# Kernel tuning notes

Hardware: AMD Instinct MI355X
Metric: run time of the kernel (lower is better)

The kernel has to match this reference:

```python
import jax, jax.numpy as jnp
import numpy as np
from jax import lax

NUM_STATES = 1024
NUM_OBS = 512
BATCH = 64
SEQ = 128


def setup_inputs() -> dict:
    key = jax.random.key(0)
    k1, k2, k3, k4 = jax.random.split(key, 4)
    value = jax.random.randint(k1, (BATCH, SEQ), 0, NUM_OBS)  # int observation ids
    prior_logits = jax.random.normal(k2, (NUM_STATES,), dtype=jnp.float32)
    trans_logits = jax.random.normal(k3, (NUM_STATES, NUM_STATES), dtype=jnp.float32)
    emission_logits = jax.random.normal(k4, (NUM_STATES, NUM_OBS), dtype=jnp.float32)
    return {"value": value, "prior_logits": prior_logits,
            "trans_logits": trans_logits, "emission_logits": emission_logits}


def reference(value, prior_logits, trans_logits, emission_logits):
    # Categorical(...).logits in torch is log-normalized: logits - logsumexp(logits)
    prior_ln = jax.nn.log_softmax(prior_logits)                 # [S]
    trans_ln = jax.nn.log_softmax(trans_logits, axis=-1)        # [S_from, S_to], row-normalized
    emis_ln = jax.nn.log_softmax(emission_logits, axis=-1)      # [S, V]
    transT = trans_ln.T                                         # [S_to, S_from]

    # Per-timestep emission log-likelihoods: emis_ln[:, value] -> [S, B, T] -> [T, B, S]
    e = jnp.transpose(emis_ln[:, value], (2, 1, 0))

    alpha0 = e[0] + prior_ln                                    # [B, S]

    def step(alpha, e_t):
        # alpha_new[b, j] = e_t[b, j] + logsumexp_i(transT[j, i] + alpha[b, i])
        a = e_t + jax.nn.logsumexp(transT[None, :, :] + alpha[:, None, :], axis=2)
        return a, None

    alpha_final, _ = lax.scan(step, alpha0, e[1:])
    return jax.nn.logsumexp(alpha_final, axis=1)                # [B]
```

## Files before the change

### kernel.cpp

```cpp
#include <hip/hip_runtime.h>
#include <hip/hip_bf16.h>


typedef __attribute__((ext_vector_type(8))) short short8;
typedef __attribute__((ext_vector_type(4))) float f32x4;
typedef __attribute__((ext_vector_type(4))) float float4v;
typedef __attribute__((ext_vector_type(4))) unsigned int uint4v;
typedef __attribute__((ext_vector_type(2))) unsigned int uint2v;

#define ALBUF_OFF 0x330000
#define DEEP_WS_NEED (ALBUF_OFF + 128 * 131072)

__device__ __forceinline__ float bf2f(short x) {
  unsigned u = ((unsigned)(unsigned short)x) << 16;
  return __builtin_bit_cast(float, u);
}
__device__ __forceinline__ short f2bf(float f) {
  unsigned u = __builtin_bit_cast(unsigned, f);
  u += 0x7fffu + ((u >> 16) & 1u);
  return (short)(u >> 16);
}
__device__ __forceinline__ float waveReduceMax(float v) {
  #pragma unroll
  for (int d = 1; d < 64; d <<= 1) v = fmaxf(v, __shfl_xor(v, d, 64));
  return v;
}
__device__ __forceinline__ float waveReduceSum(float v) {
  #pragma unroll
  for (int d = 1; d < 64; d <<= 1) v += __shfl_xor(v, d, 64);
  return v;
}
__device__ __forceinline__ void store_u32_coh(unsigned* p, unsigned v) {
  asm volatile("global_store_dword %0, %1, off sc0 sc1" :: "v"(p), "v"(v) : "memory");
}
__device__ __forceinline__ unsigned load_u32_coh(const unsigned* p) {
  unsigned r;
  asm volatile("global_load_dword %0, %1, off sc0 sc1\n\ts_waitcnt vmcnt(0)"
               : "=v"(r) : "v"(p) : "memory");
  return r;
}


__global__ __launch_bounds__(256) void k_rowstat(const float* __restrict__ x,
                                                 float* __restrict__ rstat) {
  __shared__ float sm[8];
  const int row = blockIdx.x;
  const float* p = x + row * 1024;
  const int tid = threadIdx.x;
  float m = -1e30f;
  for (int i = tid; i < 1024; i += 256) m = fmaxf(m, p[i]);
  m = waveReduceMax(m);
  if ((tid & 63) == 0) sm[tid >> 6] = m;
  __syncthreads();
  m = fmaxf(fmaxf(sm[0], sm[1]), fmaxf(sm[2], sm[3]));
  float s = 0.f;
  for (int i = tid; i < 1024; i += 256) s += __expf(p[i] - m);
  s = waveReduceSum(s);
  if ((tid & 63) == 0) sm[4 + (tid >> 6)] = s;
  __syncthreads();
  if (tid == 0) {
    float tot = sm[4] + sm[5] + sm[6] + sm[7];
    rstat[row * 2] = m;
    rstat[row * 2 + 1] = 1.0f / tot;
  }
}

__global__ __launch_bounds__(256) void k_fillP(const float* __restrict__ trans,
                                               const float* __restrict__ rstat,
                                               short* __restrict__ P_frag) {
  __shared__ float st[512];
  const int w = blockIdx.x, tid = threadIdx.x;
  for (int kk = 0; kk < 32; ++kk) {
    for (int idx = tid; idx < 512; idx += 256) {
      int il = idx >> 4, jl = idx & 15;
      int i = kk * 32 + il, j = w * 16 + jl;
      float m = rstat[i * 2], invs = rstat[i * 2 + 1];
      st[idx] = __expf(trans[i * 1024 + j] - m) * invs;
    }
    __syncthreads();
    for (int idx = tid; idx < 512; idx += 256) {
      int lane = idx >> 3, e = idx & 7;
      int il = ((lane >> 4) & 3) * 8 + e, jl = lane & 15;
      P_frag[w * 16384 + kk * 512 + idx] = f2bf(st[il * 16 + jl]);
    }
    __syncthreads();
  }
}

__global__ __launch_bounds__(256) void k_emis(const float* __restrict__ x,
                                              short* __restrict__ o) {
  __shared__ float sm[8];
  const int row = blockIdx.x;
  const float* p = x + row * 512;
  const int tid = threadIdx.x;
  float m = -1e30f;
  for (int i = tid; i < 512; i += 256) m = fmaxf(m, p[i]);
  m = waveReduceMax(m);
  if ((tid & 63) == 0) sm[tid >> 6] = m;
  __syncthreads();
  m = fmaxf(fmaxf(sm[0], sm[1]), fmaxf(sm[2], sm[3]));
  float s = 0.f;
  for (int i = tid; i < 512; i += 256) s += __expf(p[i] - m);
  s = waveReduceSum(s);
  if ((tid & 63) == 0) sm[4 + (tid >> 6)] = s;
  __syncthreads();
  float invs = 512.0f / (sm[4] + sm[5] + sm[6] + sm[7]);
  for (int i = tid; i < 512; i += 256)
    o[i * 1024 + row] = f2bf(__expf(p[i] - m) * invs);
}

__global__ __launch_bounds__(256) void k_prior(const float* __restrict__ x,
                                               float* __restrict__ o) {
  __shared__ float sm[8];
  const int tid = threadIdx.x;
  float m = -1e30f;
  for (int i = tid; i < 1024; i += 256) m = fmaxf(m, x[i]);
  m = waveReduceMax(m);
  if ((tid & 63) == 0) sm[tid >> 6] = m;
  __syncthreads();
  m = fmaxf(fmaxf(sm[0], sm[1]), fmaxf(sm[2], sm[3]));
  float s = 0.f;
  for (int i = tid; i < 1024; i += 256) s += __expf(x[i] - m);
  s = waveReduceSum(s);
  if ((tid & 63) == 0) sm[4 + (tid >> 6)] = s;
  __syncthreads();
  float invs = 1.0f / (sm[4] + sm[5] + sm[6] + sm[7]);
  for (int i = tid; i < 1024; i += 256) o[i] = __expf(x[i] - m) * invs;
}


#define PL(KK, OFF) asm volatile("global_load_dwordx4 %0, %1, off offset:" #OFF " sc0 sc1" \
                                 : "=v"(u[KK]) : "v"(arow) : "memory")
#define PL_ALL() do { \
  PL(0,0);    PL(1,64);   PL(2,128);  PL(3,192);  PL(4,256);  PL(5,320);  PL(6,384);  PL(7,448); \
  PL(8,512);  PL(9,576);  PL(10,640); PL(11,704); PL(12,768); PL(13,832); PL(14,896); PL(15,960); \
  PL(16,1024);PL(17,1088);PL(18,1152);PL(19,1216);PL(20,1280);PL(21,1344);PL(22,1408);PL(23,1472); \
  PL(24,1536);PL(25,1600);PL(26,1664);PL(27,1728);PL(28,1792);PL(29,1856);PL(30,1920);PL(31,1984); \
  asm volatile("s_waitcnt vmcnt(0)" ::: "memory"); \
  __builtin_amdgcn_sched_barrier(0); \
} while (0)

#define SENTINEL_OK(ok) do { \
  unsigned bad = 0; \
  _Pragma("unroll") \
  for (int kk = 0; kk < 32; ++kk) bad |= (u[kk].x | u[kk].y | u[kk].z | u[kk].w); \
  ok = __all((int)((bad & 0x80008000u) == 0u)); \
} while (0)

template <bool DEEP>
__global__ __launch_bounds__(256, 1) void hmm_main(
    const int* __restrict__ value, const float* __restrict__ prior_p,
    const short* __restrict__ P_frag, const short* __restrict__ emisT,
    short* __restrict__ albuf, unsigned int* __restrict__ flg,
    float* __restrict__ out) {
  __shared__ unsigned short v_lds[128 * 16];

  const int bx = blockIdx.x;
  const int d = bx & 3;
  const int m = bx >> 2;
  const int tid = threadIdx.x;
  const int lane = tid & 63;
  const int wid = tid >> 6;
  const int wv = m * 4 + wid;
  const int bl = lane & 15;
  const int kg = lane >> 4;
  const int j0 = m * 64 + wid * 16 + kg * 4;

  unsigned* flgd = flg + d * 8192;

  short8 pf[32];
  {
    const short8* pfsrc = (const short8*)(P_frag + (m * 4 + wid) * 16384) + lane;
    #pragma unroll
    for (int kk = 0; kk < 32; ++kk) pf[kk] = pfsrc[kk * 64];
  }
  for (int i = tid; i < 2048; i += 256) {
    int bli = i >> 7, tt = i & 127;
    v_lds[tt * 16 + bli] = (unsigned short)value[(d * 16 + bli) * 128 + tt];
  }
  __syncthreads();

  {
    float4v pr = *(const float4v*)(prior_p + j0);
    int obs = (int)v_lds[0 * 16 + bl];
    uint2v e0 = *(const uint2v*)(emisT + obs * 1024 + j0);
    float E0 = bf2f((short)(e0.x & 0xffff)), E1 = bf2f((short)(e0.x >> 16));
    float E2 = bf2f((short)(e0.y & 0xffff)), E3 = bf2f((short)(e0.y >> 16));
    unsigned b01 = ((unsigned)(unsigned short)f2bf(pr.x * E0)) |
                   ((unsigned)(unsigned short)f2bf(pr.y * E1) << 16);
    unsigned b23 = ((unsigned)(unsigned short)f2bf(pr.z * E2)) |
                   ((unsigned)(unsigned short)f2bf(pr.w * E3) << 16);
    uint2v ov = { b01, b23 };
    short* wout = albuf + (size_t)(d * 16 + bl) * 1024 + j0;
    asm volatile("global_store_dwordx2 %0, %1, off sc0 sc1" :: "v"(wout), "v"(ov) : "memory");
    if (!DEEP) asm volatile("s_waitcnt vmcnt(0)" ::: "memory");
    if (lane == 0) store_u32_coh(&flgd[0 * 64 + wv], 1u);
  }

  uint2v ef;
  {
    int obs = (int)v_lds[1 * 16 + bl];
    ef = *(const uint2v*)(emisT + obs * 1024 + j0);
  }

  for (int t = 1; t < 128; ++t) {
    {
      const unsigned* fp = flgd + (t - 1) * 64 + lane;
      int tries = 0;
      while (true) {
        unsigned f = load_u32_coh(fp);
        if (__all((int)(f == (unsigned)t))) break;
        if (++tries > (1 << 17)) break;
      }
    }

    size_t slot_in = DEEP ? (size_t)(t - 1) : (size_t)((t - 1) & 1);
    const short* arow = albuf + slot_in * 65536 + (size_t)(d * 16 + bl) * 1024 + kg * 8;
    uint4v u[32];
    PL_ALL();
    if (DEEP) {
      int ok, tries = 0;
      SENTINEL_OK(ok);
      while (!ok) {
        if (++tries > (1 << 17)) break;
        PL_ALL();
        SENTINEL_OK(ok);
      }
    }

    f32x4 acc0 = {0.f, 0.f, 0.f, 0.f}, acc1 = {0.f, 0.f, 0.f, 0.f};
    #pragma unroll
    for (int kk = 0; kk < 32; kk += 2) {
      acc0 = __builtin_amdgcn_mfma_f32_16x16x32_bf16(
          pf[kk], __builtin_bit_cast(short8, u[kk]), acc0, 0, 0, 0);
      acc1 = __builtin_amdgcn_mfma_f32_16x16x32_bf16(
          pf[kk + 1], __builtin_bit_cast(short8, u[kk + 1]), acc1, 0, 0, 0);
    }

    float E0 = bf2f((short)(ef.x & 0xffff)), E1 = bf2f((short)(ef.x >> 16));
    float E2 = bf2f((short)(ef.y & 0xffff)), E3 = bf2f((short)(ef.y >> 16));
    unsigned b01 = ((unsigned)(unsigned short)f2bf((acc0[0] + acc1[0]) * E0)) |
                   ((unsigned)(unsigned short)f2bf((acc0[1] + acc1[1]) * E1) << 16);
    unsigned b23 = ((unsigned)(unsigned short)f2bf((acc0[2] + acc1[2]) * E2)) |
                   ((unsigned)(unsigned short)f2bf((acc0[3] + acc1[3]) * E3) << 16);
    uint2v ov = { b01, b23 };
    size_t slot_out = DEEP ? (size_t)t : (size_t)(t & 1);
    short* wout = albuf + slot_out * 65536 + (size_t)(d * 16 + bl) * 1024 + j0;
    asm volatile("global_store_dwordx2 %0, %1, off sc0 sc1" :: "v"(wout), "v"(ov) : "memory");
    if (!DEEP) asm volatile("s_waitcnt vmcnt(0)" ::: "memory");
    if (lane == 0) store_u32_coh(&flgd[t * 64 + wv], (unsigned)(t + 1));

    if (t < 127) {
      int obs = (int)v_lds[(t + 1) * 16 + bl];
      ef = *(const uint2v*)(emisT + obs * 1024 + j0);
    }
  }

  if (m != 0) return;
  {
    const unsigned* fp = flgd + 127 * 64 + lane;
    int tries = 0;
    while (true) {
      unsigned f = load_u32_coh(fp);
      if (__all((int)(f == 128u))) break;
      if (++tries > (1 << 17)) break;
    }
    size_t slotF = DEEP ? (size_t)127 : (size_t)1;
    const short* arow = albuf + slotF * 65536 + (size_t)(d * 16 + bl) * 1024 + kg * 8;
    uint4v u[32];
    PL_ALL();
    if (DEEP) {
      int ok, tries2 = 0;
      SENTINEL_OK(ok);
      while (!ok) {
        if (++tries2 > (1 << 17)) break;
        PL_ALL();
        SENTINEL_OK(ok);
      }
    }
    float s = 0.f;
    #pragma unroll
    for (int kk = 0; kk < 32; ++kk) {
      #pragma unroll
      for (int q = 0; q < 4; ++q) {
        unsigned w = (q == 0) ? u[kk].x : (q == 1) ? u[kk].y : (q == 2) ? u[kk].z : u[kk].w;
        s += bf2f((short)(w & 0xffff));
        s += bf2f((short)(w >> 16));
      }
    }
    s += __shfl_xor(s, 16, 64);
    s += __shfl_xor(s, 32, 64);
    if (wid == 0 && lane < 16)
      out[d * 16 + lane] = logf(s) - 798.5055520050569f;
  }
}

extern "C" void kernel_launch(void* const* d_in, const int* in_sizes, int n_in,
                              void* d_out, int out_size, void* d_ws, size_t ws_size,
                              hipStream_t stream) {
  const int* value = (const int*)d_in[0];
  const float* prior = (const float*)d_in[1];
  const float* trans = (const float*)d_in[2];
  const float* emis = (const float*)d_in[3];
  char* ws = (char*)d_ws;
  short* P_frag = (short*)(ws + 0x000000);
  short* emisT = (short*)(ws + 0x200000);
  float* prior_p = (float*)(ws + 0x300000);
  float* rstat = (float*)(ws + 0x304000);
  unsigned* flg = (unsigned*)(ws + 0x310000);
  short* albuf = (short*)(ws + ALBUF_OFF);
  float* out = (float*)d_out;

  k_rowstat<<<1024, 256, 0, stream>>>(trans, rstat);
  k_fillP<<<64, 256, 0, stream>>>(trans, rstat, P_frag);
  k_emis<<<1024, 256, 0, stream>>>(emis, emisT);
  k_prior<<<1, 256, 0, stream>>>(prior, prior_p);
  if (ws_size >= (size_t)DEEP_WS_NEED) {
    hmm_main<true><<<64, 256, 0, stream>>>(value, prior_p, P_frag, emisT, albuf, flg, out);
  } else {
    hmm_main<false><<<64, 256, 0, stream>>>(value, prior_p, P_frag, emisT, albuf, flg, out);
  }
}
```

Baseline: 857.8 us.

## Halve grid, double per-wave columns, process alpha chunks as they arrive

The grid drops from 64 to 32 blocks, so each wave now computes 32 output states instead of 16. Half of the transition fragments stay in registers and the other half are staged in LDS. In the deep-buffer path the flag spin-wait is removed. Instead, the 2 KB alpha row is loaded in eight chunks, and each chunk is consumed by MFMA as soon as its sentinel check passes, so polling overlaps with compute and cross-block synchronisation needs fewer participants. The cost is more serial MFMA work per wave, LDS reads for half the weights, and a possibly longer critical path per timestep.

```diff
diff --git a/kernel.cpp b/kernel.cpp
--- a/kernel.cpp
+++ b/kernel.cpp
@@ -131,20 +131,41 @@
 
 #define PL(KK, OFF) asm volatile("global_load_dwordx4 %0, %1, off offset:" #OFF " sc0 sc1" \
                                  : "=v"(u[KK]) : "v"(arow) : "memory")
-#define PL_ALL() do { \
-  PL(0,0);    PL(1,64);   PL(2,128);  PL(3,192);  PL(4,256);  PL(5,320);  PL(6,384);  PL(7,448); \
-  PL(8,512);  PL(9,576);  PL(10,640); PL(11,704); PL(12,768); PL(13,832); PL(14,896); PL(15,960); \
-  PL(16,1024);PL(17,1088);PL(18,1152);PL(19,1216);PL(20,1280);PL(21,1344);PL(22,1408);PL(23,1472); \
-  PL(24,1536);PL(25,1600);PL(26,1664);PL(27,1728);PL(28,1792);PL(29,1856);PL(30,1920);PL(31,1984); \
+#define ISS(P, O0, O1, O2, O3) \
+  if (pending & (1u << P)) { PL(4*P+0, O0); PL(4*P+1, O1); PL(4*P+2, O2); PL(4*P+3, O3); }
+#define ISS_ALL() do { \
+  ISS(0,0,64,128,192)       ISS(1,256,320,384,448)   ISS(2,512,576,640,704) \
+  ISS(3,768,832,896,960)    ISS(4,1024,1088,1152,1216) ISS(5,1280,1344,1408,1472) \
+  ISS(6,1536,1600,1664,1728) ISS(7,1792,1856,1920,1984) \
   asm volatile("s_waitcnt vmcnt(0)" ::: "memory"); \
   __builtin_amdgcn_sched_barrier(0); \
 } while (0)
-
-#define SENTINEL_OK(ok) do { \
-  unsigned bad = 0; \
-  _Pragma("unroll") \
-  for (int kk = 0; kk < 32; ++kk) bad |= (u[kk].x | u[kk].y | u[kk].z | u[kk].w); \
+#define POK(P, ok) do { \
+  unsigned bad = u[4*P].x | u[4*P].y | u[4*P].z | u[4*P].w \
+               | u[4*P+1].x | u[4*P+1].y | u[4*P+1].z | u[4*P+1].w \
+               | u[4*P+2].x | u[4*P+2].y | u[4*P+2].z | u[4*P+2].w \
+               | u[4*P+3].x | u[4*P+3].y | u[4*P+3].z | u[4*P+3].w; \
   ok = __all((int)((bad & 0x80008000u) == 0u)); \
+} while (0)
+#define PROC(P) do { \
+  if (pending & (1u << P)) { \
+    int ok; POK(P, ok); \
+    if (ok) { \
+      short8 b0 = __builtin_bit_cast(short8, u[4*P+0]); \
+      short8 b1 = __builtin_bit_cast(short8, u[4*P+1]); \
+      short8 b2 = __builtin_bit_cast(short8, u[4*P+2]); \
+      short8 b3 = __builtin_bit_cast(short8, u[4*P+3]); \
+      acc00 = __builtin_amdgcn_mfma_f32_16x16x32_bf16(pf0[4*P+0], b0, acc00, 0, 0, 0); \
+      acc10 = __builtin_amdgcn_mfma_f32_16x16x32_bf16(pl8[plb + (4*P+0)*64], b0, acc10, 0, 0, 0); \
+      acc01 = __builtin_amdgcn_mfma_f32_16x16x32_bf16(pf0[4*P+1], b1, acc01, 0, 0, 0); \
+      acc11 = __builtin_amdgcn_mfma_f32_16x16x32_bf16(pl8[plb + (4*P+1)*64], b1, acc11, 0, 0, 0); \
+      acc00 = __builtin_amdgcn_mfma_f32_16x16x32_bf16(pf0[4*P+2], b2, acc00, 0, 0, 0); \
+      acc10 = __builtin_amdgcn_mfma_f32_16x16x32_bf16(pl8[plb + (4*P+2)*64], b2, acc10, 0, 0, 0); \
+      acc01 = __builtin_amdgcn_mfma_f32_16x16x32_bf16(pf0[4*P+3], b3, acc01, 0, 0, 0); \
+      acc11 = __builtin_amdgcn_mfma_f32_16x16x32_bf16(pl8[plb + (4*P+3)*64], b3, acc11, 0, 0, 0); \
+      pending &= ~(1u << P); \
+    } \
+  } \
 } while (0)
 
 template <bool DEEP>
@@ -153,6 +174,7 @@
     const short* __restrict__ P_frag, const short* __restrict__ emisT,
     short* __restrict__ albuf, unsigned int* __restrict__ flg,
     float* __restrict__ out) {
+  __shared__ __align__(16) short8 pl8[4 * 32 * 64];
   __shared__ unsigned short v_lds[128 * 16];
 
   const int bx = blockIdx.x;
@@ -161,18 +183,20 @@
   const int tid = threadIdx.x;
   const int lane = tid & 63;
   const int wid = tid >> 6;
-  const int wv = m * 4 + wid;
   const int bl = lane & 15;
   const int kg = lane >> 4;
-  const int j0 = m * 64 + wid * 16 + kg * 4;
-
-  unsigned* flgd = flg + d * 8192;
-
-  short8 pf[32];
+  const int j0 = m * 128 + wid * 32 + kg * 4;
+  const int plb = wid * 2048 + lane;
+
+  short8 pf0[32];
   {
-    const short8* pfsrc = (const short8*)(P_frag + (m * 4 + wid) * 16384) + lane;
+    const short8* s0 = (const short8*)(P_frag + (8 * m + 2 * wid) * 16384) + lane;
+    const short8* s1 = (const short8*)(P_frag + (8 * m + 2 * wid + 1) * 16384) + lane;
     #pragma unroll
-    for (int kk = 0; kk < 32; ++kk) pf[kk] = pfsrc[kk * 64];
+    for (int kk = 0; kk < 32; ++kk) {
+      pf0[kk] = s0[kk * 64];
+      pl8[plb + kk * 64] = s1[kk * 64];
+    }
   }
   for (int i = tid; i < 2048; i += 256) {
     int bli = i >> 7, tt = i & 127;
@@ -181,31 +205,39 @@
   __syncthreads();
 
   {
-    float4v pr = *(const float4v*)(prior_p + j0);
     int obs = (int)v_lds[0 * 16 + bl];
+    float4v pr0 = *(const float4v*)(prior_p + j0);
+    float4v pr1 = *(const float4v*)(prior_p + j0 + 16);
     uint2v e0 = *(const uint2v*)(emisT + obs * 1024 + j0);
-    float E0 = bf2f((short)(e0.x & 0xffff)), E1 = bf2f((short)(e0.x >> 16));
-    float E2 = bf2f((short)(e0.y & 0xffff)), E3 = bf2f((short)(e0.y >> 16));
-    unsigned b01 = ((unsigned)(unsigned short)f2bf(pr.x * E0)) |
-                   ((unsigned)(unsigned short)f2bf(pr.y * E1) << 16);
-    unsigned b23 = ((unsigned)(unsigned short)f2bf(pr.z * E2)) |
-                   ((unsigned)(unsigned short)f2bf(pr.w * E3) << 16);
-    uint2v ov = { b01, b23 };
+    uint2v e1 = *(const uint2v*)(emisT + obs * 1024 + j0 + 16);
+    unsigned a01 = ((unsigned)(unsigned short)f2bf(pr0.x * bf2f((short)(e0.x & 0xffff)))) |
+                   ((unsigned)(unsigned short)f2bf(pr0.y * bf2f((short)(e0.x >> 16))) << 16);
+    unsigned a23 = ((unsigned)(unsigned short)f2bf(pr0.z * bf2f((short)(e0.y & 0xffff)))) |
+                   ((unsigned)(unsigned short)f2bf(pr0.w * bf2f((short)(e0.y >> 16))) << 16);
+    unsigned b01 = ((unsigned)(unsigned short)f2bf(pr1.x * bf2f((short)(e1.x & 0xffff)))) |
+                   ((unsigned)(unsigned short)f2bf(pr1.y * bf2f((short)(e1.x >> 16))) << 16);
+    unsigned b23 = ((unsigned)(unsigned short)f2bf(pr1.z * bf2f((short)(e1.y & 0xffff)))) |
+                   ((unsigned)(unsigned short)f2bf(pr1.w * bf2f((short)(e1.y >> 16))) << 16);
+    uint2v ov0 = { a01, a23 }, ov1 = { b01, b23 };
     short* wout = albuf + (size_t)(d * 16 + bl) * 1024 + j0;
-    asm volatile("global_store_dwordx2 %0, %1, off sc0 sc1" :: "v"(wout), "v"(ov) : "memory");
-    if (!DEEP) asm volatile("s_waitcnt vmcnt(0)" ::: "memory");
-    if (lane == 0) store_u32_coh(&flgd[0 * 64 + wv], 1u);
-  }
-
-  uint2v ef;
+    asm volatile("global_store_dwordx2 %0, %1, off sc0 sc1" :: "v"(wout), "v"(ov0) : "memory");
+    asm volatile("global_store_dwordx2 %0, %1, off offset:32 sc0 sc1" :: "v"(wout), "v"(ov1) : "memory");
+    if (!DEEP) {
+      asm volatile("s_waitcnt vmcnt(0)" ::: "memory");
+      if (lane == 0) store_u32_coh(&flg[d * 4096 + 0 * 32 + m * 4 + wid], 1u);
+    }
+  }
+
+  uint2v ef0, ef1;
   {
     int obs = (int)v_lds[1 * 16 + bl];
-    ef = *(const uint2v*)(emisT + obs * 1024 + j0);
+    ef0 = *(const uint2v*)(emisT + obs * 1024 + j0);
+    ef1 = *(const uint2v*)(emisT + obs * 1024 + j0 + 16);
   }
 
   for (int t = 1; t < 128; ++t) {
-    {
-      const unsigned* fp = flgd + (t - 1) * 64 + lane;
+    if (!DEEP) {
+      const unsigned* fp = flg + d * 4096 + (t - 1) * 32 + (lane & 31);
       int tries = 0;
       while (true) {
         unsigned f = load_u32_coh(fp);
@@ -217,67 +249,73 @@
     size_t slot_in = DEEP ? (size_t)(t - 1) : (size_t)((t - 1) & 1);
     const short* arow = albuf + slot_in * 65536 + (size_t)(d * 16 + bl) * 1024 + kg * 8;
     uint4v u[32];
-    PL_ALL();
-    if (DEEP) {
-      int ok, tries = 0;
-      SENTINEL_OK(ok);
-      while (!ok) {
-        if (++tries > (1 << 17)) break;
-        PL_ALL();
-        SENTINEL_OK(ok);
-      }
-    }
-
-    f32x4 acc0 = {0.f, 0.f, 0.f, 0.f}, acc1 = {0.f, 0.f, 0.f, 0.f};
-    #pragma unroll
-    for (int kk = 0; kk < 32; kk += 2) {
-      acc0 = __builtin_amdgcn_mfma_f32_16x16x32_bf16(
-          pf[kk], __builtin_bit_cast(short8, u[kk]), acc0, 0, 0, 0);
-      acc1 = __builtin_amdgcn_mfma_f32_16x16x32_bf16(
-          pf[kk + 1], __builtin_bit_cast(short8, u[kk + 1]), acc1, 0, 0, 0);
-    }
-
-    float E0 = bf2f((short)(ef.x & 0xffff)), E1 = bf2f((short)(ef.x >> 16));
-    float E2 = bf2f((short)(ef.y & 0xffff)), E3 = bf2f((short)(ef.y >> 16));
-    unsigned b01 = ((unsigned)(unsigned short)f2bf((acc0[0] + acc1[0]) * E0)) |
-                   ((unsigned)(unsigned short)f2bf((acc0[1] + acc1[1]) * E1) << 16);
-    unsigned b23 = ((unsigned)(unsigned short)f2bf((acc0[2] + acc1[2]) * E2)) |
-                   ((unsigned)(unsigned short)f2bf((acc0[3] + acc1[3]) * E3) << 16);
-    uint2v ov = { b01, b23 };
+    f32x4 acc00 = {0.f,0.f,0.f,0.f}, acc01 = {0.f,0.f,0.f,0.f};
+    f32x4 acc10 = {0.f,0.f,0.f,0.f}, acc11 = {0.f,0.f,0.f,0.f};
+    unsigned pending = 0xFFu;
+    int sweeps = 0;
+    do {
+      ISS_ALL();
+      PROC(0); PROC(1); PROC(2); PROC(3);
+      PROC(4); PROC(5); PROC(6); PROC(7);
+    } while (pending && ++sweeps < (1 << 15));
+
+    unsigned a01 = ((unsigned)(unsigned short)f2bf((acc00[0] + acc01[0]) * bf2f((short)(ef0.x & 0xffff)))) |
+                   ((unsigned)(unsigned short)f2bf((acc00[1] + acc01[1]) * bf2f((short)(ef0.x >> 16))) << 16);
+    unsigned a23 = ((unsigned)(unsigned short)f2bf((acc00[2] + acc01[2]) * bf2f((short)(ef0.y & 0xffff)))) |
+                   ((unsigned)(unsigned short)f2bf((acc00[3] + acc01[3]) * bf2f((short)(ef0.y >> 16))) << 16);
+    unsigned b01 = ((unsigned)(unsigned short)f2bf((acc10[0] + acc11[0]) * bf2f((short)(ef1.x & 0xffff)))) |
+                   ((unsigned)(unsigned short)f2bf((acc10[1] + acc11[1]) * bf2f((short)(ef1.x >> 16))) << 16);
+    unsigned b23 = ((unsigned)(unsigned short)f2bf((acc10[2] + acc11[2]) * bf2f((short)(ef1.y & 0xffff)))) |
+                   ((unsigned)(unsigned short)f2bf((acc10[3] + acc11[3]) * bf2f((short)(ef1.y >> 16))) << 16);
+    uint2v ov0 = { a01, a23 }, ov1 = { b01, b23 };
     size_t slot_out = DEEP ? (size_t)t : (size_t)(t & 1);
     short* wout = albuf + slot_out * 65536 + (size_t)(d * 16 + bl) * 1024 + j0;
-    asm volatile("global_store_dwordx2 %0, %1, off sc0 sc1" :: "v"(wout), "v"(ov) : "memory");
-    if (!DEEP) asm volatile("s_waitcnt vmcnt(0)" ::: "memory");
-    if (lane == 0) store_u32_coh(&flgd[t * 64 + wv], (unsigned)(t + 1));
+    asm volatile("global_store_dwordx2 %0, %1, off sc0 sc1" :: "v"(wout), "v"(ov0) : "memory");
+    asm volatile("global_store_dwordx2 %0, %1, off offset:32 sc0 sc1" :: "v"(wout), "v"(ov1) : "memory");
+    if (!DEEP) {
+      asm volatile("s_waitcnt vmcnt(0)" ::: "memory");
+      if (lane == 0) store_u32_coh(&flg[d * 4096 + t * 32 + m * 4 + wid], (unsigned)(t + 1));
+    }
 
     if (t < 127) {
       int obs = (int)v_lds[(t + 1) * 16 + bl];
-      ef = *(const uint2v*)(emisT + obs * 1024 + j0);
-    }
-  }
-
-  if (m != 0) return;
+      ef0 = *(const uint2v*)(emisT + obs * 1024 + j0);
+      ef1 = *(const uint2v*)(emisT + obs * 1024 + j0 + 16);
+    }
+  }
+
+  if (m != 0 || wid != 0) return;
   {
-    const unsigned* fp = flgd + 127 * 64 + lane;
-    int tries = 0;
-    while (true) {
-      unsigned f = load_u32_coh(fp);
-      if (__all((int)(f == 128u))) break;
-      if (++tries > (1 << 17)) break;
+    if (!DEEP) {
+      const unsigned* fp = flg + d * 4096 + 127 * 32 + (lane & 31);
+      int tries = 0;
+      while (true) {
+        unsigned f = load_u32_coh(fp);
+        if (__all((int)(f == 128u))) break;
+        if (++tries > (1 << 17)) break;
+      }
     }
     size_t slotF = DEEP ? (size_t)127 : (size_t)1;
     const short* arow = albuf + slotF * 65536 + (size_t)(d * 16 + bl) * 1024 + kg * 8;
     uint4v u[32];
-    PL_ALL();
-    if (DEEP) {
-      int ok, tries2 = 0;
-      SENTINEL_OK(ok);
-      while (!ok) {
-        if (++tries2 > (1 << 17)) break;
-        PL_ALL();
-        SENTINEL_OK(ok);
+    unsigned pending = 0xFFu;
+    int sweeps = 0;
+    do {
+      ISS_ALL();
+      if (DEEP) {
+        int ok;
+        POK(0, ok); if (ok) pending &= ~1u;
+        POK(1, ok); if (ok) pending &= ~2u;
+        POK(2, ok); if (ok) pending &= ~4u;
+        POK(3, ok); if (ok) pending &= ~8u;
+        POK(4, ok); if (ok) pending &= ~16u;
+        POK(5, ok); if (ok) pending &= ~32u;
+        POK(6, ok); if (ok) pending &= ~64u;
+        POK(7, ok); if (ok) pending &= ~128u;
+      } else {
+        pending = 0u;
       }
-    }
+    } while (pending && ++sweeps < (1 << 15));
     float s = 0.f;
     #pragma unroll
     for (int kk = 0; kk < 32; ++kk) {
@@ -290,7 +328,7 @@
     }
     s += __shfl_xor(s, 16, 64);
     s += __shfl_xor(s, 32, 64);
-    if (wid == 0 && lane < 16)
+    if (lane < 16)
       out[d * 16 + lane] = logf(s) - 798.5055520050569f;
   }
 }
@@ -316,8 +354,8 @@
   k_emis<<<1024, 256, 0, stream>>>(emis, emisT);
   k_prior<<<1, 256, 0, stream>>>(prior, prior_p);
   if (ws_size >= (size_t)DEEP_WS_NEED) {
-    hmm_main<true><<<64, 256, 0, stream>>>(value, prior_p, P_frag, emisT, albuf, flg, out);
+    hmm_main<true><<<32, 256, 0, stream>>>(value, prior_p, P_frag, emisT, albuf, flg, out);
   } else {
-    hmm_main<false><<<64, 256, 0, stream>>>(value, prior_p, P_frag, emisT, albuf, flg, out);
-  }
-}
+    hmm_main<false><<<32, 256, 0, stream>>>(value, prior_p, P_frag, emisT, albuf, flg, out);
+  }
+}
```

After: 903.6 us. +5.3%, slower.

## Use per-block flags with workgroup barrier and selective reload of sentinel chunks

Applied to the files above, without the earlier changes.

Cuts the flag granularity from one per wave to one per workgroup. Each block now syncs its four waves with s_barrier before thread 0 publishes the step flag, so pollers read 16 flags instead of 64. In the DEEP path the alpha row is first read with ordinary cached loads, and only the 16-byte chunks still holding the sentinel are re-fetched with coherent loads. This is meant to reduce coherent-load traffic and polling cost, but it adds an intra-block barrier every step, and the non-DEEP path now waits on each load in turn rather than batching them.

```diff
diff --git a/kernel.cpp b/kernel.cpp
--- a/kernel.cpp
+++ b/kernel.cpp
@@ -36,6 +36,12 @@
 __device__ __forceinline__ unsigned load_u32_coh(const unsigned* p) {
   unsigned r;
   asm volatile("global_load_dword %0, %1, off sc0 sc1\n\ts_waitcnt vmcnt(0)"
+               : "=v"(r) : "v"(p) : "memory");
+  return r;
+}
+__device__ __forceinline__ uint4v load_b16_uc(const short* p) {
+  uint4v r;
+  asm volatile("global_load_dwordx4 %0, %1, off sc0 sc1\n\ts_waitcnt vmcnt(0)"
                : "=v"(r) : "v"(p) : "memory");
   return r;
 }
@@ -129,24 +135,6 @@
 }
 
 
-#define PL(KK, OFF) asm volatile("global_load_dwordx4 %0, %1, off offset:" #OFF " sc0 sc1" \
-                                 : "=v"(u[KK]) : "v"(arow) : "memory")
-#define PL_ALL() do { \
-  PL(0,0);    PL(1,64);   PL(2,128);  PL(3,192);  PL(4,256);  PL(5,320);  PL(6,384);  PL(7,448); \
-  PL(8,512);  PL(9,576);  PL(10,640); PL(11,704); PL(12,768); PL(13,832); PL(14,896); PL(15,960); \
-  PL(16,1024);PL(17,1088);PL(18,1152);PL(19,1216);PL(20,1280);PL(21,1344);PL(22,1408);PL(23,1472); \
-  PL(24,1536);PL(25,1600);PL(26,1664);PL(27,1728);PL(28,1792);PL(29,1856);PL(30,1920);PL(31,1984); \
-  asm volatile("s_waitcnt vmcnt(0)" ::: "memory"); \
-  __builtin_amdgcn_sched_barrier(0); \
-} while (0)
-
-#define SENTINEL_OK(ok) do { \
-  unsigned bad = 0; \
-  _Pragma("unroll") \
-  for (int kk = 0; kk < 32; ++kk) bad |= (u[kk].x | u[kk].y | u[kk].z | u[kk].w); \
-  ok = __all((int)((bad & 0x80008000u) == 0u)); \
-} while (0)
-
 template <bool DEEP>
 __global__ __launch_bounds__(256, 1) void hmm_main(
     const int* __restrict__ value, const float* __restrict__ prior_p,
@@ -161,12 +149,10 @@
   const int tid = threadIdx.x;
   const int lane = tid & 63;
   const int wid = tid >> 6;
-  const int wv = m * 4 + wid;
   const int bl = lane & 15;
   const int kg = lane >> 4;
   const int j0 = m * 64 + wid * 16 + kg * 4;
-
-  unsigned* flgd = flg + d * 8192;
+  unsigned* flgd = flg + d * 2048;
 
   short8 pf[32];
   {
@@ -194,7 +180,9 @@
     short* wout = albuf + (size_t)(d * 16 + bl) * 1024 + j0;
     asm volatile("global_store_dwordx2 %0, %1, off sc0 sc1" :: "v"(wout), "v"(ov) : "memory");
     if (!DEEP) asm volatile("s_waitcnt vmcnt(0)" ::: "memory");
-    if (lane == 0) store_u32_coh(&flgd[0 * 64 + wv], 1u);
+    __builtin_amdgcn_sched_barrier(0);
+    __builtin_amdgcn_s_barrier();
+    if (tid == 0) store_u32_coh(&flgd[0 * 16 + m], 1u);
   }
 
   uint2v ef;
@@ -205,7 +193,7 @@
 
   for (int t = 1; t < 128; ++t) {
     {
-      const unsigned* fp = flgd + (t - 1) * 64 + lane;
+      const unsigned* fp = flgd + (t - 1) * 16 + bl;
       int tries = 0;
       while (true) {
         unsigned f = load_u32_coh(fp);
@@ -217,15 +205,29 @@
     size_t slot_in = DEEP ? (size_t)(t - 1) : (size_t)((t - 1) & 1);
     const short* arow = albuf + slot_in * 65536 + (size_t)(d * 16 + bl) * 1024 + kg * 8;
     uint4v u[32];
-    PL_ALL();
     if (DEEP) {
-      int ok, tries = 0;
-      SENTINEL_OK(ok);
-      while (!ok) {
-        if (++tries > (1 << 17)) break;
-        PL_ALL();
-        SENTINEL_OK(ok);
+      const short8* ab8 = (const short8*)arow;
+      #pragma unroll
+      for (int kk = 0; kk < 32; ++kk) u[kk] = __builtin_bit_cast(uint4v, ab8[kk * 4]);
+      unsigned bad = 0;
+      #pragma unroll
+      for (int kk = 0; kk < 32; ++kk) bad |= (u[kk].x | u[kk].y | u[kk].z | u[kk].w);
+      int allok = __all((int)((bad & 0x80008000u) == 0u));
+      int tries = 0;
+      while (!allok && ++tries < (1 << 17)) {
+        #pragma unroll
+        for (int kk = 0; kk < 32; ++kk) {
+          unsigned bk = (u[kk].x | u[kk].y | u[kk].z | u[kk].w) & 0x80008000u;
+          if (bk) u[kk] = load_b16_uc(arow + kk * 32);
+        }
+        bad = 0;
+        #pragma unroll
+        for (int kk = 0; kk < 32; ++kk) bad |= (u[kk].x | u[kk].y | u[kk].z | u[kk].w);
+        allok = __all((int)((bad & 0x80008000u) == 0u));
       }
+    } else {
+      #pragma unroll
+      for (int kk = 0; kk < 32; ++kk) u[kk] = load_b16_uc(arow + kk * 32);
     }
 
     f32x4 acc0 = {0.f, 0.f, 0.f, 0.f}, acc1 = {0.f, 0.f, 0.f, 0.f};
@@ -248,7 +250,9 @@
     short* wout = albuf + slot_out * 65536 + (size_t)(d * 16 + bl) * 1024 + j0;
     asm volatile("global_store_dwordx2 %0, %1, off sc0 sc1" :: "v"(wout), "v"(ov) : "memory");
     if (!DEEP) asm volatile("s_waitcnt vmcnt(0)" ::: "memory");
-    if (lane == 0) store_u32_coh(&flgd[t * 64 + wv], (unsigned)(t + 1));
+    __builtin_amdgcn_sched_barrier(0);
+    __builtin_amdgcn_s_barrier();
+    if (tid == 0) store_u32_coh(&flgd[t * 16 + m], (unsigned)(t + 1));
 
     if (t < 127) {
       int obs = (int)v_lds[(t + 1) * 16 + bl];
@@ -256,9 +260,9 @@
     }
   }
 
-  if (m != 0) return;
+  if (m != 0 || wid != 0) return;
   {
-    const unsigned* fp = flgd + 127 * 64 + lane;
+    const unsigned* fp = flgd + 127 * 16 + bl;
     int tries = 0;
     while (true) {
       unsigned f = load_u32_coh(fp);
@@ -268,15 +272,29 @@
     size_t slotF = DEEP ? (size_t)127 : (size_t)1;
     const short* arow = albuf + slotF * 65536 + (size_t)(d * 16 + bl) * 1024 + kg * 8;
     uint4v u[32];
-    PL_ALL();
     if (DEEP) {
-      int ok, tries2 = 0;
-      SENTINEL_OK(ok);
-      while (!ok) {
-        if (++tries2 > (1 << 17)) break;
-        PL_ALL();
-        SENTINEL_OK(ok);
+      const short8* ab8 = (const short8*)arow;
+      #pragma unroll
+      for (int kk = 0; kk < 32; ++kk) u[kk] = __builtin_bit_cast(uint4v, ab8[kk * 4]);
+      unsigned bad = 0;
+      #pragma unroll
+      for (int kk = 0; kk < 32; ++kk) bad |= (u[kk].x | u[kk].y | u[kk].z | u[kk].w);
+      int allok = __all((int)((bad & 0x80008000u) == 0u));
+      int tries2 = 0;
+      while (!allok && ++tries2 < (1 << 17)) {
+        #pragma unroll
+        for (int kk = 0; kk < 32; ++kk) {
+          unsigned bk = (u[kk].x | u[kk].y | u[kk].z | u[kk].w) & 0x80008000u;
+          if (bk) u[kk] = load_b16_uc(arow + kk * 32);
+        }
+        bad = 0;
+        #pragma unroll
+        for (int kk = 0; kk < 32; ++kk) bad |= (u[kk].x | u[kk].y | u[kk].z | u[kk].w);
+        allok = __all((int)((bad & 0x80008000u) == 0u));
       }
+    } else {
+      #pragma unroll
+      for (int kk = 0; kk < 32; ++kk) u[kk] = load_b16_uc(arow + kk * 32);
     }
     float s = 0.f;
     #pragma unroll
@@ -290,7 +308,7 @@
     }
     s += __shfl_xor(s, 16, 64);
     s += __shfl_xor(s, 32, 64);
-    if (wid == 0 && lane < 16)
+    if (lane < 16)
       out[d * 16 + lane] = logf(s) - 798.5055520050569f;
   }
 }
```

After: 731.6 us. 14.7% less time.
